# Optimization experiments

Hardware: AMD Instinct MI355X
Metric: run time of the kernel (lower is better)

The kernel has to match this reference:

```python
import jax, jax.numpy as jnp
import numpy as np

B, C, L, H = 8, 1024, 1024, 16
GROUPS = 32
EPS = 1e-5


def setup_inputs() -> dict:
    key = jax.random.key(0)
    ks = jax.random.split(key, 5)
    return {
        "x": jax.random.normal(ks[0], (B, C, L), dtype=jnp.float32),
        "norm_w": jnp.ones((C,), dtype=jnp.float32),
        "norm_b": jnp.zeros((C,), dtype=jnp.float32),
        "qkv_w": jax.random.normal(ks[1], (3 * C, C), dtype=jnp.float32) * (1.0 / np.sqrt(C)),
        "qkv_b": jax.random.normal(ks[2], (3 * C,), dtype=jnp.float32) * 0.02,
        "proj_w": jax.random.normal(ks[3], (C, C), dtype=jnp.float32) * (1.0 / np.sqrt(C)),
        "proj_b": jax.random.normal(ks[4], (C,), dtype=jnp.float32) * 0.02,
    }


def _group_norm(x, w, b):
    # x: [B, C, L]; GroupNorm over (channels-in-group, length)
    bs, c, l = x.shape
    xg = x.reshape(bs, GROUPS, c // GROUPS, l)
    mean = jnp.mean(xg, axis=(2, 3), keepdims=True)
    var = jnp.var(xg, axis=(2, 3), keepdims=True)
    xn = ((xg - mean) * jax.lax.rsqrt(var + EPS)).reshape(bs, c, l)
    return xn * w[None, :, None] + b[None, :, None]


def reference(x, norm_w, norm_b, qkv_w, qkv_b, proj_w, proj_b):
    b, c, l = x.shape
    ch = c // H  # per-head channels
    x_norm = _group_norm(x, norm_w, norm_b)
    # 1x1 conv == channel matmul: [B, 3C, L]
    qkv = jnp.einsum('oc,bcl->bol', qkv_w, x_norm) + qkv_b[None, :, None]
    # torch layout: reshape(bs*H, 3*ch, L) then split -> per-head [q; k; v]
    qkv = qkv.reshape(b * H, 3 * ch, l)
    q, k, v = qkv[:, :ch], qkv[:, ch:2 * ch], qkv[:, 2 * ch:]
    scale = 1.0 / np.sqrt(np.sqrt(ch))
    # explicit [b*H, L, L] score matrix, softmax in fp32 (matches .float())
    weight = jnp.einsum('bct,bcs->bts', q * scale, k * scale)
    weight = jax.nn.softmax(weight.astype(jnp.float32), axis=-1)
    a = jnp.einsum('bts,bcs->bct', weight, v.astype(jnp.float32))
    h = a.reshape(b, c, l).astype(x.dtype)
    h = jnp.einsum('oc,bcl->bol', proj_w, h) + proj_b[None, :, None]
    return x_norm + h  # tortoise_norm=False branch
```

## Files before the change

kernel.cpp:

```cpp
#include <hip/hip_runtime.h>
#include <cstdint>
#include <cstddef>

#define B_   8
#define C_   1024
#define L_   1024
#define H_   16
#define CH_  64
#define NG_  32
#define CPG_ 32

typedef __bf16 bf16;
typedef _Float16 f16;
typedef bf16  bf16x8 __attribute__((ext_vector_type(8)));
typedef bf16  bf16x4 __attribute__((ext_vector_type(4)));
typedef f16   f16x4  __attribute__((ext_vector_type(4)));
typedef f16   f16x2  __attribute__((ext_vector_type(2)));
typedef float f32x4  __attribute__((ext_vector_type(4)));

#define QSCALE 0.1803368801111203f

__device__ __forceinline__ void async_cp16(void* lds, const void* g) {
  __builtin_amdgcn_global_load_lds((__attribute__((address_space(1))) void*)g,
                                   (__attribute__((address_space(3))) void*)lds,
                                   16, 0, 0);
}

__device__ __forceinline__ f16x2 pk_f16(float a, float b) {
  return __builtin_bit_cast(f16x2, __builtin_amdgcn_cvt_pkrtz(a, b));
}

__device__ __forceinline__ int sw64(int r, int c) {
  return r * 64 + ((c ^ (r & 7)) << 3);
}

__global__ __launch_bounds__(256) void cvt_bf16_kernel(const float* __restrict__ src,
                                                       bf16* __restrict__ dst, int n4) {
  int i = blockIdx.x * 256 + threadIdx.x;
  if (i < n4) {
    float4 f = reinterpret_cast<const float4*>(src)[i];
    bf16x4 o;
    o[0] = (bf16)f.x; o[1] = (bf16)f.y; o[2] = (bf16)f.z; o[3] = (bf16)f.w;
    reinterpret_cast<bf16x4*>(dst)[i] = o;
  }
}

__global__ __launch_bounds__(256) void gn_stats_kernel(const float* __restrict__ x,
                                                       float* __restrict__ stats) {
  const int bg = blockIdx.x >> 3, sl = blockIdx.x & 7;
  const int tid = threadIdx.x;
  const float* xs = x + (size_t)bg * CPG_ * L_;
  const int c = tid >> 3;
  const int lbase = sl * 128 + (tid & 7) * 4;

  float s = 0.f, s2 = 0.f;
  #pragma unroll
  for (int t = 0; t < 4; t++) {
    float4 f = *reinterpret_cast<const float4*>(xs + (size_t)c * L_ + lbase + t * 32);
    s  += f.x + f.y + f.z + f.w;
    s2 += f.x * f.x + f.y * f.y + f.z * f.z + f.w * f.w;
  }
  __shared__ float rs[256], rs2[256];
  rs[tid] = s; rs2[tid] = s2;
  __syncthreads();
  for (int d = 128; d > 0; d >>= 1) {
    if (tid < d) { rs[tid] += rs[tid + d]; rs2[tid] += rs2[tid + d]; }
    __syncthreads();
  }
  if (tid == 0) {
    atomicAdd(&stats[bg * 2],     rs[0]);
    atomicAdd(&stats[bg * 2 + 1], rs2[0]);
  }
}

__global__ __launch_bounds__(256) void gn_apply_kernel(const float* __restrict__ x,
                                                       const float* __restrict__ gw,
                                                       const float* __restrict__ gb,
                                                       const float* __restrict__ stats,
                                                       bf16* __restrict__ xnb,
                                                       bf16* __restrict__ xT) {
  const int bg = blockIdx.x >> 2, l0 = (blockIdx.x & 3) * 256;
  const int b = bg >> 5, g = bg & 31;
  const int tid = threadIdx.x;
  const float* xs = x + (size_t)bg * CPG_ * L_;

  const float mean = stats[bg * 2] * (1.f / 32768.f);
  const float var  = stats[bg * 2 + 1] * (1.f / 32768.f) - mean * mean;
  const float inv  = rsqrtf(var + 1e-5f);

  __shared__ float tile[CPG_][257];
  #pragma unroll 4
  for (int c = 0; c < CPG_; c++) {
    const int gc = g * CPG_ + c;
    const float y = (xs[(size_t)c * L_ + l0 + tid] - mean) * inv * gw[gc] + gb[gc];
    xnb[(size_t)(b * C_ + gc) * L_ + l0 + tid] = (bf16)y;
    tile[c][tid] = y;
  }
  __syncthreads();
  const int c2 = tid & 31, lw = tid >> 5;
  #pragma unroll 4
  for (int jj = 0; jj < 32; jj++) {
    const int l = l0 + jj * 8 + lw;
    xT[(size_t)(b * L_ + l) * C_ + g * CPG_ + c2] = (bf16)tile[c2][jj * 8 + lw];
  }
}

__device__ __forceinline__ void gemm128_bt(const bf16* __restrict__ A,
                                           const bf16* __restrict__ Bt,
                                           int lda, int ldb, int K,
                                           int m0, int n0,
                                           bf16* As, bf16* Bs,
                                           f32x4 acc[4][4]) {
  const int tid  = threadIdx.x;
  const int wave = tid >> 6, lane = tid & 63;
  const int wm = (wave >> 1) * 64, wn = (wave & 1) * 64;
  const int l4 = lane & 15, quad = lane >> 4;
  const int rsub = lane >> 3;
  const int csrc = (((lane & 7) ^ rsub) << 3);

  const bf16* ga = A  + (size_t)(m0 + rsub) * lda + csrc;
  const bf16* gb = Bt + (size_t)(n0 + rsub) * ldb + csrc;

  for (int k0 = 0; k0 < K; k0 += 64) {
    __syncthreads();
    #pragma unroll
    for (int i = wave; i < 16; i += 4) {
      async_cp16(As + i * 512, ga + (size_t)(i * 8) * lda + k0);
      async_cp16(Bs + i * 512, gb + (size_t)(i * 8) * ldb + k0);
    }
    __syncthreads();

    #pragma unroll
    for (int kk = 0; kk < 2; kk++) {
      bf16x8 af[4], bfv[4];
      #pragma unroll
      for (int i = 0; i < 4; i++) {
        af[i] = *reinterpret_cast<const bf16x8*>(As + sw64(wm + i * 16 + l4, kk * 4 + quad));
      }
      #pragma unroll
      for (int j = 0; j < 4; j++) {
        bfv[j] = *reinterpret_cast<const bf16x8*>(Bs + sw64(wn + j * 16 + l4, kk * 4 + quad));
      }
      #pragma unroll
      for (int i = 0; i < 4; i++) {
        #pragma unroll
        for (int j = 0; j < 4; j++) {
          acc[i][j] = __builtin_amdgcn_mfma_f32_16x16x32_bf16(af[i], bfv[j], acc[i][j], 0, 0, 0);
        }
      }
    }
  }
}

__global__ __launch_bounds__(256) void qkv_gemm_kernel(const bf16* __restrict__ Wq,
                                                       const bf16* __restrict__ xT,
                                                       const float* __restrict__ bias,
                                                       bf16* __restrict__ qT,
                                                       bf16* __restrict__ kT,
                                                       f16* __restrict__ vB) {
  __shared__ bf16 As[128 * 64], Bs[128 * 64];
  const int bi = blockIdx.z;
  const int m0 = blockIdx.y * 128, n0 = blockIdx.x * 128;

  f32x4 acc[4][4];
  #pragma unroll
  for (int i = 0; i < 4; i++) {
    #pragma unroll
    for (int j = 0; j < 4; j++) { acc[i][j] = (f32x4){0.f, 0.f, 0.f, 0.f}; }
  }

  gemm128_bt(Wq, xT + (size_t)bi * L_ * C_, C_, C_, C_, m0, n0, As, Bs, acc);

  const int tid = threadIdx.x;
  const int wave = tid >> 6, lane = tid & 63;
  const int wm = (wave >> 1) * 64, wn = (wave & 1) * 64;
  const int l4 = lane & 15, quad = lane >> 4;

  #pragma unroll
  for (int i = 0; i < 4; i++) {
    const int ob = m0 + wm + i * 16 + quad * 4;
    const int h = ob / 192, r = ob % 192;
    const int sec = r >> 6, c = r & 63;
    float bb[4];
    #pragma unroll
    for (int rg = 0; rg < 4; rg++) { bb[rg] = bias[ob + rg]; }
    #pragma unroll
    for (int j = 0; j < 4; j++) {
      const int l = n0 + wn + j * 16 + l4;
      f32x4 a = acc[i][j];
      if (sec == 2) {
        const int e = l & 63, g64 = l >> 6;
        #pragma unroll
        for (int rg = 0; rg < 4; rg++) {
          const int cc = c + rg;
          const int ep = ((((e >> 2) ^ cc) & 15) << 2) | (e & 3);
          vB[(size_t)((bi * H_ + h) * CH_ + cc) * L_ + (g64 << 6) + ep] =
              (f16)(a[rg] + bb[rg]);
        }
      } else {
        const float sc = (sec == 0) ? QSCALE : 1.0f;
        bf16* dst = (sec == 0 ? qT : kT) + (size_t)((bi * H_ + h) * L_ + l) * CH_ + c;
        bf16x4 o;
        #pragma unroll
        for (int rg = 0; rg < 4; rg++) { o[rg] = (bf16)((a[rg] + bb[rg]) * sc); }
        *reinterpret_cast<bf16x4*>(dst) = o;
      }
    }
  }
}

__global__ __launch_bounds__(256) void attn_kernel(const bf16* __restrict__ qT,
                                                   const bf16* __restrict__ kT,
                                                   const f16* __restrict__ vB,
                                                   bf16* __restrict__ aT) {
  const int tid = threadIdx.x, wave = tid >> 6, lane = tid & 63;
  const int l4 = lane & 15, quad = lane >> 4;
  const int rsub = lane >> 3;
  const int csrc = ((lane & 7) ^ rsub) << 3;

  __shared__ bf16 qs[128 * 64];
  __shared__ bf16 ks[2][64 * 64];
  __shared__ f16  vs[2][64 * 64];

  const f16x2 one2 = {(f16)1.f, (f16)1.f};

  for (int rep = 0; rep < 2; rep++) {
    const int tile = blockIdx.x + rep * 512;
    const int t0 = (tile & 7) * 128;
    const int hb = tile >> 3;
    const bf16* q = qT + (size_t)hb * L_ * CH_;
    const bf16* k = kT + (size_t)hb * L_ * CH_;
    const f16*  v = vB + (size_t)hb * CH_ * L_;

    __syncthreads();
    {
      const bf16* gq = q + (size_t)t0 * CH_;
      #pragma unroll
      for (int i = wave; i < 16; i += 4) {
        async_cp16((char*)qs + i * 1024, gq + (i * 8 + rsub) * 64 + csrc);
      }
      #pragma unroll
      for (int i = wave; i < 8; i += 4) {
        async_cp16((char*)ks[0] + i * 1024, k + (size_t)(i * 8 + rsub) * 64 + csrc);
        async_cp16((char*)vs[0] + i * 1024, v + (size_t)(i * 8 + rsub) * L_ + ((lane & 7) << 3));
      }
    }
    __syncthreads();

    bf16x8 bq0[2], bq1[2];
    #pragma unroll
    for (int u = 0; u < 2; u++) {
      bq0[u] = *reinterpret_cast<const bf16x8*>(qs + sw64(wave * 32 + u * 16 + l4, quad));
      bq1[u] = *reinterpret_cast<const bf16x8*>(qs + sw64(wave * 32 + u * 16 + l4, quad + 4));
    }

    f32x4 oacc[2][4];
    float m_s[2], l_s[2];
    #pragma unroll
    for (int u = 0; u < 2; u++) {
      #pragma unroll
      for (int ct = 0; ct < 4; ct++) { oacc[u][ct] = (f32x4){0.f, 0.f, 0.f, 0.f}; }
      m_s[u] = -1e30f; l_s[u] = 0.f;
    }

    for (int it = 0; it < 16; it++) {
      const int cur = it & 1;
      if (it < 15) {
        const int s1 = (it + 1) * 64;
        const bf16* gk = k + (size_t)s1 * CH_;
        const f16*  gv = v + s1;
        #pragma unroll
        for (int i = wave; i < 8; i += 4) {
          async_cp16((char*)ks[cur ^ 1] + i * 1024, gk + (size_t)(i * 8 + rsub) * 64 + csrc);
          async_cp16((char*)vs[cur ^ 1] + i * 1024, gv + (size_t)(i * 8 + rsub) * L_ + ((lane & 7) << 3));
        }
      }
      const bf16* ksc = ks[cur];
      const f16*  vsc = vs[cur];

      f32x4 st[2][4];
      #pragma unroll
      for (int j = 0; j < 4; j++) {
        const bf16x8 ak0 = *reinterpret_cast<const bf16x8*>(ksc + sw64(j * 16 + l4, quad));
        const bf16x8 ak1 = *reinterpret_cast<const bf16x8*>(ksc + sw64(j * 16 + l4, quad + 4));
        #pragma unroll
        for (int u = 0; u < 2; u++) {
          f32x4 z = (f32x4){0.f, 0.f, 0.f, 0.f};
          z = __builtin_amdgcn_mfma_f32_16x16x32_bf16(ak0, bq0[u], z, 0, 0, 0);
          z = __builtin_amdgcn_mfma_f32_16x16x32_bf16(ak1, bq1[u], z, 0, 0, 0);
          st[u][j] = z;
        }
      }

      f16x2 plo[2][4], phi[2][4];
      float alpha[2];
      #pragma unroll
      for (int u = 0; u < 2; u++) {
        float mx = fmaxf(fmaxf(st[u][0][0], st[u][0][1]), fmaxf(st[u][0][2], st[u][0][3]));
        #pragma unroll
        for (int j = 1; j < 4; j++) {
          mx = fmaxf(mx, fmaxf(fmaxf(st[u][j][0], st[u][j][1]), fmaxf(st[u][j][2], st[u][j][3])));
        }
        mx = fmaxf(mx, __shfl_xor(mx, 16));
        mx = fmaxf(mx, __shfl_xor(mx, 32));
        const float mn = fmaxf(m_s[u], mx);
        alpha[u] = __builtin_amdgcn_exp2f(m_s[u] - mn);
        m_s[u] = mn;
        float sm = 0.f;
        #pragma unroll
        for (int j = 0; j < 4; j++) {
          const float p0 = __builtin_amdgcn_exp2f(st[u][j][0] - mn);
          const float p1 = __builtin_amdgcn_exp2f(st[u][j][1] - mn);
          const float p2 = __builtin_amdgcn_exp2f(st[u][j][2] - mn);
          const float p3 = __builtin_amdgcn_exp2f(st[u][j][3] - mn);
          plo[u][j] = pk_f16(p0, p1);
          phi[u][j] = pk_f16(p2, p3);
          sm = __builtin_amdgcn_fdot2(plo[u][j], one2, sm, false);
          sm = __builtin_amdgcn_fdot2(phi[u][j], one2, sm, false);
        }
        sm += __shfl_xor(sm, 16);
        sm += __shfl_xor(sm, 32);
        l_s[u] = l_s[u] * alpha[u] + sm;
      }

      if (__any(alpha[0] != 1.0f || alpha[1] != 1.0f)) {
        #pragma unroll
        for (int u = 0; u < 2; u++) {
          float ar[4];
          #pragma unroll
          for (int r = 0; r < 4; r++) { ar[r] = __shfl(alpha[u], quad * 4 + r); }
          #pragma unroll
          for (int ct = 0; ct < 4; ct++) {
            #pragma unroll
            for (int r = 0; r < 4; r++) { oacc[u][ct][r] *= ar[r]; }
          }
        }
      }

      #pragma unroll
      for (int ct = 0; ct < 4; ct++) {
        const int c = ct * 16 + l4;
        #pragma unroll
        for (int j = 0; j < 4; j++) {
          const f16x4 vb = *reinterpret_cast<const f16x4*>(
              vsc + c * 64 + (((4 * j + quad) ^ l4) << 2));
          #pragma unroll
          for (int u = 0; u < 2; u++) {
            const f16x4 av = __builtin_shufflevector(plo[u][j], phi[u][j], 0, 1, 2, 3);
            oacc[u][ct] = __builtin_amdgcn_mfma_f32_16x16x16f16(av, vb, oacc[u][ct], 0, 0, 0);
          }
        }
      }
      __syncthreads();
    }

    const int bi = hb >> 4, h = hb & 15;
    #pragma unroll
    for (int u = 0; u < 2; u++) {
      float linv[4];
      #pragma unroll
      for (int r = 0; r < 4; r++) { linv[r] = 1.f / __shfl(l_s[u], quad * 4 + r); }
      #pragma unroll
      for (int ct = 0; ct < 4; ct++) {
        #pragma unroll
        for (int r = 0; r < 4; r++) {
          const int t = t0 + wave * 32 + u * 16 + quad * 4 + r;
          const int c = h * CH_ + ct * 16 + l4;
          aT[(size_t)(bi * L_ + t) * C_ + c] = (bf16)(oacc[u][ct][r] * linv[r]);
        }
      }
    }
  }
}

__global__ __launch_bounds__(256) void proj_gemm_kernel(const bf16* __restrict__ Wp,
                                                        const bf16* __restrict__ aT,
                                                        const float* __restrict__ bias,
                                                        const bf16* __restrict__ xnb,
                                                        float* __restrict__ out) {
  __shared__ bf16 As[128 * 64], Bs[128 * 64];
  const int bi = blockIdx.z;
  const int m0 = blockIdx.y * 128, n0 = blockIdx.x * 128;

  f32x4 acc[4][4];
  #pragma unroll
  for (int i = 0; i < 4; i++) {
    #pragma unroll
    for (int j = 0; j < 4; j++) { acc[i][j] = (f32x4){0.f, 0.f, 0.f, 0.f}; }
  }

  gemm128_bt(Wp, aT + (size_t)bi * L_ * C_, C_, C_, C_, m0, n0, As, Bs, acc);

  const int tid = threadIdx.x;
  const int wave = tid >> 6, lane = tid & 63;
  const int wm = (wave >> 1) * 64, wn = (wave & 1) * 64;
  const int l4 = lane & 15, quad = lane >> 4;

  #pragma unroll
  for (int i = 0; i < 4; i++) {
    const int ob = m0 + wm + i * 16 + quad * 4;
    float bb[4];
    #pragma unroll
    for (int rg = 0; rg < 4; rg++) { bb[rg] = bias[ob + rg]; }
    #pragma unroll
    for (int j = 0; j < 4; j++) {
      const int l = n0 + wn + j * 16 + l4;
      #pragma unroll
      for (int rg = 0; rg < 4; rg++) {
        const size_t idx = (size_t)(bi * C_ + ob + rg) * L_ + l;
        out[idx] = acc[i][j][rg] + bb[rg] + (float)xnb[idx];
      }
    }
  }
}

extern "C" void kernel_launch(void* const* d_in, const int* in_sizes, int n_in,
                              void* d_out, int out_size, void* d_ws, size_t ws_size,
                              hipStream_t stream) {
  (void)in_sizes; (void)n_in; (void)out_size; (void)ws_size;
  const float* x      = (const float*)d_in[0];
  const float* norm_w = (const float*)d_in[1];
  const float* norm_b = (const float*)d_in[2];
  const float* qkv_w  = (const float*)d_in[3];
  const float* qkv_b  = (const float*)d_in[4];
  const float* proj_w = (const float*)d_in[5];
  const float* proj_b = (const float*)d_in[6];
  float* out = (float*)d_out;

  char* w = (char*)d_ws;
  auto alloc = [&](size_t bytes) {
    char* p = w;
    w += (bytes + 255) & ~(size_t)255;
    return p;
  };
  bf16*  xnb   = (bf16*)alloc((size_t)B_ * C_ * L_ * 2);
  bf16*  xT    = (bf16*)alloc((size_t)B_ * L_ * C_ * 2);
  bf16*  wq    = (bf16*)alloc((size_t)3 * C_ * C_ * 2);
  bf16*  wp    = (bf16*)alloc((size_t)C_ * C_ * 2);
  bf16*  qT    = (bf16*)alloc((size_t)B_ * H_ * L_ * CH_ * 2);
  bf16*  kT    = (bf16*)alloc((size_t)B_ * H_ * L_ * CH_ * 2);
  f16*   vB    = (f16*)alloc((size_t)B_ * H_ * CH_ * L_ * 2);
  bf16*  aTb   = (bf16*)alloc((size_t)B_ * L_ * C_ * 2);
  float* stats = (float*)alloc((size_t)B_ * NG_ * 2 * 4);

  (void)hipMemsetAsync(stats, 0, (size_t)B_ * NG_ * 2 * 4, stream);
  cvt_bf16_kernel<<<(3 * C_ * C_ / 4) / 256, 256, 0, stream>>>(qkv_w, wq, 3 * C_ * C_ / 4);
  cvt_bf16_kernel<<<(C_ * C_ / 4) / 256, 256, 0, stream>>>(proj_w, wp, C_ * C_ / 4);
  gn_stats_kernel<<<B_ * NG_ * 8, 256, 0, stream>>>(x, stats);
  gn_apply_kernel<<<B_ * NG_ * 4, 256, 0, stream>>>(x, norm_w, norm_b, stats, xnb, xT);
  qkv_gemm_kernel<<<dim3(L_ / 128, 3 * C_ / 128, B_), 256, 0, stream>>>(wq, xT, qkv_b, qT, kT, vB);
  attn_kernel<<<512, 256, 0, stream>>>(qT, kT, vB, aTb);
  proj_gemm_kernel<<<dim3(L_ / 128, C_ / 128, B_), 256, 0, stream>>>(wp, aTb, proj_b, xnb, out);
}
```

Baseline: 297.0 us.

## Raise attention occupancy: one tile per block, shared LDS, MFMA row sums

The attention kernel now launches 1024 blocks, each handling a single tile instead of looping over two, and sets launch bounds to allow 4 blocks per CU. LDS is cut to 32 KB by placing Q in the second K/V double buffer and reading it into registers before the loop. The softmax row sum is now accumulated through an extra MFMA against a ones vector rather than fdot2 plus cross-lane shuffles, which removes the final shuffle for the normaliser. The aim is more resident waves to hide latency and fewer VALU and shuffle ops, at the cost of extra MFMA work and register-pressure limits from the launch bound.

```diff
diff --git a/kernel.cpp b/kernel.cpp
--- a/kernel.cpp
+++ b/kernel.cpp
@@ -209,165 +209,166 @@
   }
 }
 
-__global__ __launch_bounds__(256) void attn_kernel(const bf16* __restrict__ qT,
-                                                   const bf16* __restrict__ kT,
-                                                   const f16* __restrict__ vB,
-                                                   bf16* __restrict__ aT) {
+__global__ __launch_bounds__(256, 4) void attn_kernel(const bf16* __restrict__ qT,
+                                                      const bf16* __restrict__ kT,
+                                                      const f16* __restrict__ vB,
+                                                      bf16* __restrict__ aT) {
   const int tid = threadIdx.x, wave = tid >> 6, lane = tid & 63;
   const int l4 = lane & 15, quad = lane >> 4;
   const int rsub = lane >> 3;
   const int csrc = ((lane & 7) ^ rsub) << 3;
 
-  __shared__ bf16 qs[128 * 64];
-  __shared__ bf16 ks[2][64 * 64];
-  __shared__ f16  vs[2][64 * 64];
-
-  const f16x2 one2 = {(f16)1.f, (f16)1.f};
-
-  for (int rep = 0; rep < 2; rep++) {
-    const int tile = blockIdx.x + rep * 512;
-    const int t0 = (tile & 7) * 128;
-    const int hb = tile >> 3;
-    const bf16* q = qT + (size_t)hb * L_ * CH_;
-    const bf16* k = kT + (size_t)hb * L_ * CH_;
-    const f16*  v = vB + (size_t)hb * CH_ * L_;
-
-    __syncthreads();
-    {
-      const bf16* gq = q + (size_t)t0 * CH_;
-      #pragma unroll
-      for (int i = wave; i < 16; i += 4) {
-        async_cp16((char*)qs + i * 1024, gq + (i * 8 + rsub) * 64 + csrc);
-      }
-      #pragma unroll
-      for (int i = wave; i < 8; i += 4) {
-        async_cp16((char*)ks[0] + i * 1024, k + (size_t)(i * 8 + rsub) * 64 + csrc);
-        async_cp16((char*)vs[0] + i * 1024, v + (size_t)(i * 8 + rsub) * L_ + ((lane & 7) << 3));
-      }
-    }
-    __syncthreads();
-
-    bf16x8 bq0[2], bq1[2];
+  __shared__ char smem[32768];
+
+  const int tile = blockIdx.x;
+  const int t0 = (tile & 7) * 128;
+  const int hb = tile >> 3;
+  const bf16* q = qT + (size_t)hb * L_ * CH_;
+  const bf16* k = kT + (size_t)hb * L_ * CH_;
+  const f16*  v = vB + (size_t)hb * CH_ * L_;
+
+  {
+    const bf16* gq = q + (size_t)t0 * CH_;
+    #pragma unroll
+    for (int i = wave; i < 16; i += 4) {
+      async_cp16(smem + 16384 + i * 1024, gq + (i * 8 + rsub) * 64 + csrc);
+    }
+    #pragma unroll
+    for (int i = wave; i < 8; i += 4) {
+      async_cp16(smem + i * 1024, k + (size_t)(i * 8 + rsub) * 64 + csrc);
+      async_cp16(smem + 8192 + i * 1024, v + (size_t)(i * 8 + rsub) * L_ + ((lane & 7) << 3));
+    }
+  }
+  __syncthreads();
+
+  bf16x8 bq0[2], bq1[2];
+  {
+    const bf16* qs = (const bf16*)(smem + 16384);
     #pragma unroll
     for (int u = 0; u < 2; u++) {
       bq0[u] = *reinterpret_cast<const bf16x8*>(qs + sw64(wave * 32 + u * 16 + l4, quad));
       bq1[u] = *reinterpret_cast<const bf16x8*>(qs + sw64(wave * 32 + u * 16 + l4, quad + 4));
     }
-
-    f32x4 oacc[2][4];
-    float m_s[2], l_s[2];
+  }
+  __syncthreads();
+
+  f32x4 oacc[2][4];
+  f32x4 lacc[2];
+  float m_s[2];
+  #pragma unroll
+  for (int u = 0; u < 2; u++) {
+    #pragma unroll
+    for (int ct = 0; ct < 4; ct++) { oacc[u][ct] = (f32x4){0.f, 0.f, 0.f, 0.f}; }
+    lacc[u] = (f32x4){0.f, 0.f, 0.f, 0.f};
+    m_s[u] = -1e30f;
+  }
+
+  const f16x4 vone = {(f16)1.f, (f16)1.f, (f16)1.f, (f16)1.f};
+
+  for (int it = 0; it < 16; it++) {
+    const int cur = it & 1;
+    if (it < 15) {
+      const int s1 = (it + 1) * 64;
+      char* nb = smem + (cur ^ 1) * 16384;
+      const bf16* gk = k + (size_t)s1 * CH_;
+      const f16*  gv = v + s1;
+      #pragma unroll
+      for (int i = wave; i < 8; i += 4) {
+        async_cp16(nb + i * 1024, gk + (size_t)(i * 8 + rsub) * 64 + csrc);
+        async_cp16(nb + 8192 + i * 1024, gv + (size_t)(i * 8 + rsub) * L_ + ((lane & 7) << 3));
+      }
+    }
+    const bf16* ksc = (const bf16*)(smem + cur * 16384);
+    const f16*  vsc = (const f16*)(smem + cur * 16384 + 8192);
+
+    f32x4 st[2][4];
+    #pragma unroll
+    for (int j = 0; j < 4; j++) {
+      const bf16x8 ak0 = *reinterpret_cast<const bf16x8*>(ksc + sw64(j * 16 + l4, quad));
+      const bf16x8 ak1 = *reinterpret_cast<const bf16x8*>(ksc + sw64(j * 16 + l4, quad + 4));
+      #pragma unroll
+      for (int u = 0; u < 2; u++) {
+        f32x4 z = (f32x4){0.f, 0.f, 0.f, 0.f};
+        z = __builtin_amdgcn_mfma_f32_16x16x32_bf16(ak0, bq0[u], z, 0, 0, 0);
+        z = __builtin_amdgcn_mfma_f32_16x16x32_bf16(ak1, bq1[u], z, 0, 0, 0);
+        st[u][j] = z;
+      }
+    }
+
+    float alpha[2], mn[2];
     #pragma unroll
     for (int u = 0; u < 2; u++) {
-      #pragma unroll
-      for (int ct = 0; ct < 4; ct++) { oacc[u][ct] = (f32x4){0.f, 0.f, 0.f, 0.f}; }
-      m_s[u] = -1e30f; l_s[u] = 0.f;
-    }
-
-    for (int it = 0; it < 16; it++) {
-      const int cur = it & 1;
-      if (it < 15) {
-        const int s1 = (it + 1) * 64;
-        const bf16* gk = k + (size_t)s1 * CH_;
-        const f16*  gv = v + s1;
-        #pragma unroll
-        for (int i = wave; i < 8; i += 4) {
-          async_cp16((char*)ks[cur ^ 1] + i * 1024, gk + (size_t)(i * 8 + rsub) * 64 + csrc);
-          async_cp16((char*)vs[cur ^ 1] + i * 1024, gv + (size_t)(i * 8 + rsub) * L_ + ((lane & 7) << 3));
+      float mx = fmaxf(fmaxf(st[u][0][0], st[u][0][1]), fmaxf(st[u][0][2], st[u][0][3]));
+      #pragma unroll
+      for (int j = 1; j < 4; j++) {
+        mx = fmaxf(mx, fmaxf(fmaxf(st[u][j][0], st[u][j][1]), fmaxf(st[u][j][2], st[u][j][3])));
+      }
+      mx = fmaxf(mx, __shfl_xor(mx, 16));
+      mx = fmaxf(mx, __shfl_xor(mx, 32));
+      mn[u] = fmaxf(m_s[u], mx);
+      alpha[u] = __builtin_amdgcn_exp2f(m_s[u] - mn[u]);
+      m_s[u] = mn[u];
+    }
+
+    if (__any(alpha[0] != 1.0f || alpha[1] != 1.0f)) {
+      #pragma unroll
+      for (int u = 0; u < 2; u++) {
+        float ar[4];
+        #pragma unroll
+        for (int r = 0; r < 4; r++) { ar[r] = __shfl(alpha[u], quad * 4 + r); }
+        #pragma unroll
+        for (int ct = 0; ct < 4; ct++) {
+          #pragma unroll
+          for (int r = 0; r < 4; r++) { oacc[u][ct][r] *= ar[r]; }
         }
-      }
-      const bf16* ksc = ks[cur];
-      const f16*  vsc = vs[cur];
-
-      f32x4 st[2][4];
+        #pragma unroll
+        for (int r = 0; r < 4; r++) { lacc[u][r] *= ar[r]; }
+      }
+    }
+
+    f16x4 pa[2][4];
+    #pragma unroll
+    for (int u = 0; u < 2; u++) {
       #pragma unroll
       for (int j = 0; j < 4; j++) {
-        const bf16x8 ak0 = *reinterpret_cast<const bf16x8*>(ksc + sw64(j * 16 + l4, quad));
-        const bf16x8 ak1 = *reinterpret_cast<const bf16x8*>(ksc + sw64(j * 16 + l4, quad + 4));
+        const float p0 = __builtin_amdgcn_exp2f(st[u][j][0] - mn[u]);
+        const float p1 = __builtin_amdgcn_exp2f(st[u][j][1] - mn[u]);
+        const float p2 = __builtin_amdgcn_exp2f(st[u][j][2] - mn[u]);
+        const float p3 = __builtin_amdgcn_exp2f(st[u][j][3] - mn[u]);
+        pa[u][j] = __builtin_shufflevector(pk_f16(p0, p1), pk_f16(p2, p3), 0, 1, 2, 3);
+        lacc[u] = __builtin_amdgcn_mfma_f32_16x16x16f16(pa[u][j], vone, lacc[u], 0, 0, 0);
+      }
+    }
+
+    #pragma unroll
+    for (int ct = 0; ct < 4; ct++) {
+      const int c = ct * 16 + l4;
+      #pragma unroll
+      for (int j = 0; j < 4; j++) {
+        const f16x4 vb = *reinterpret_cast<const f16x4*>(
+            vsc + c * 64 + (((4 * j + quad) ^ l4) << 2));
         #pragma unroll
         for (int u = 0; u < 2; u++) {
-          f32x4 z = (f32x4){0.f, 0.f, 0.f, 0.f};
-          z = __builtin_amdgcn_mfma_f32_16x16x32_bf16(ak0, bq0[u], z, 0, 0, 0);
-          z = __builtin_amdgcn_mfma_f32_16x16x32_bf16(ak1, bq1[u], z, 0, 0, 0);
-          st[u][j] = z;
+          oacc[u][ct] = __builtin_amdgcn_mfma_f32_16x16x16f16(pa[u][j], vb, oacc[u][ct], 0, 0, 0);
         }
       }
-
-      f16x2 plo[2][4], phi[2][4];
-      float alpha[2];
-      #pragma unroll
-      for (int u = 0; u < 2; u++) {
-        float mx = fmaxf(fmaxf(st[u][0][0], st[u][0][1]), fmaxf(st[u][0][2], st[u][0][3]));
-        #pragma unroll
-        for (int j = 1; j < 4; j++) {
-          mx = fmaxf(mx, fmaxf(fmaxf(st[u][j][0], st[u][j][1]), fmaxf(st[u][j][2], st[u][j][3])));
-        }
-        mx = fmaxf(mx, __shfl_xor(mx, 16));
-        mx = fmaxf(mx, __shfl_xor(mx, 32));
-        const float mn = fmaxf(m_s[u], mx);
-        alpha[u] = __builtin_amdgcn_exp2f(m_s[u] - mn);
-        m_s[u] = mn;
-        float sm = 0.f;
-        #pragma unroll
-        for (int j = 0; j < 4; j++) {
-          const float p0 = __builtin_amdgcn_exp2f(st[u][j][0] - mn);
-          const float p1 = __builtin_amdgcn_exp2f(st[u][j][1] - mn);
-          const float p2 = __builtin_amdgcn_exp2f(st[u][j][2] - mn);
-          const float p3 = __builtin_amdgcn_exp2f(st[u][j][3] - mn);
-          plo[u][j] = pk_f16(p0, p1);
-          phi[u][j] = pk_f16(p2, p3);
-          sm = __builtin_amdgcn_fdot2(plo[u][j], one2, sm, false);
-          sm = __builtin_amdgcn_fdot2(phi[u][j], one2, sm, false);
-        }
-        sm += __shfl_xor(sm, 16);
-        sm += __shfl_xor(sm, 32);
-        l_s[u] = l_s[u] * alpha[u] + sm;
-      }
-
-      if (__any(alpha[0] != 1.0f || alpha[1] != 1.0f)) {
-        #pragma unroll
-        for (int u = 0; u < 2; u++) {
-          float ar[4];
-          #pragma unroll
-          for (int r = 0; r < 4; r++) { ar[r] = __shfl(alpha[u], quad * 4 + r); }
-          #pragma unroll
-          for (int ct = 0; ct < 4; ct++) {
-            #pragma unroll
-            for (int r = 0; r < 4; r++) { oacc[u][ct][r] *= ar[r]; }
-          }
-        }
-      }
-
-      #pragma unroll
-      for (int ct = 0; ct < 4; ct++) {
-        const int c = ct * 16 + l4;
-        #pragma unroll
-        for (int j = 0; j < 4; j++) {
-          const f16x4 vb = *reinterpret_cast<const f16x4*>(
-              vsc + c * 64 + (((4 * j + quad) ^ l4) << 2));
-          #pragma unroll
-          for (int u = 0; u < 2; u++) {
-            const f16x4 av = __builtin_shufflevector(plo[u][j], phi[u][j], 0, 1, 2, 3);
-            oacc[u][ct] = __builtin_amdgcn_mfma_f32_16x16x16f16(av, vb, oacc[u][ct], 0, 0, 0);
-          }
-        }
-      }
-      __syncthreads();
-    }
-
-    const int bi = hb >> 4, h = hb & 15;
-    #pragma unroll
-    for (int u = 0; u < 2; u++) {
-      float linv[4];
-      #pragma unroll
-      for (int r = 0; r < 4; r++) { linv[r] = 1.f / __shfl(l_s[u], quad * 4 + r); }
-      #pragma unroll
-      for (int ct = 0; ct < 4; ct++) {
-        #pragma unroll
-        for (int r = 0; r < 4; r++) {
-          const int t = t0 + wave * 32 + u * 16 + quad * 4 + r;
-          const int c = h * CH_ + ct * 16 + l4;
-          aT[(size_t)(bi * L_ + t) * C_ + c] = (bf16)(oacc[u][ct][r] * linv[r]);
-        }
+    }
+    __syncthreads();
+  }
+
+  const int bi = hb >> 4, h = hb & 15;
+  #pragma unroll
+  for (int u = 0; u < 2; u++) {
+    float linv[4];
+    #pragma unroll
+    for (int r = 0; r < 4; r++) { linv[r] = 1.f / lacc[u][r]; }
+    #pragma unroll
+    for (int ct = 0; ct < 4; ct++) {
+      #pragma unroll
+      for (int r = 0; r < 4; r++) {
+        const int t = t0 + wave * 32 + u * 16 + quad * 4 + r;
+        const int c = h * CH_ + ct * 16 + l4;
+        aT[(size_t)(bi * L_ + t) * C_ + c] = (bf16)(oacc[u][ct][r] * linv[r]);
       }
     }
   }
@@ -449,6 +450,6 @@
   gn_stats_kernel<<<B_ * NG_ * 8, 256, 0, stream>>>(x, stats);
   gn_apply_kernel<<<B_ * NG_ * 4, 256, 0, stream>>>(x, norm_w, norm_b, stats, xnb, xT);
   qkv_gemm_kernel<<<dim3(L_ / 128, 3 * C_ / 128, B_), 256, 0, stream>>>(wq, xT, qkv_b, qT, kT, vB);
-  attn_kernel<<<512, 256, 0, stream>>>(qT, kT, vB, aTb);
+  attn_kernel<<<1024, 256, 0, stream>>>(qT, kT, vB, aTb);
   proj_gemm_kernel<<<dim3(L_ / 128, C_ / 128, B_), 256, 0, stream>>>(wp, aTb, proj_b, xnb, out);
 }
```

Result: faster. 266.8 us (-10.2%).
